# Kernel optimization log

Measured on AMD Instinct MI355X. Metric: run time of the kernel, lower is better.

## Reference

```python
import jax, jax.numpy as jnp
import numpy as np

CAPACITY = 8_388_608  # 2**23, power of two -> leftmost_leaf == capacity
N_UPDATES = 1_048_576  # 2**20


def setup_inputs() -> dict:
    key = jax.random.key(0)
    k1, k2, k3 = jax.random.split(key, 3)
    # Existing tree buffer; values[1] is root, values[CAPACITY:2*CAPACITY] are leaves.
    tree_values = jax.random.uniform(k1, (2 * CAPACITY,), dtype=jnp.float32)
    # Distinct leaf indices in [0, CAPACITY): torch scatter-assign with duplicate
    # indices is nondeterministic, so the meaningful case is distinct indices.
    indices = jax.random.permutation(k2, CAPACITY)[:N_UPDATES].astype(jnp.int32)
    values = jax.random.uniform(k3, (N_UPDATES,), dtype=jnp.float32)
    return {"tree_values": tree_values, "indices": indices, "values": values}


def reference(tree_values, indices, values):
    """SegmentTree.__setitem__ with op=add: set leaves, propagate sums to root.

    Returns the updated (2*capacity,) tree buffer.
    """
    capacity = tree_values.shape[0] // 2  # static python int
    depth = int(capacity).bit_length() - 1  # log2(capacity) levels to the root
    # _index_to_leaf: with power-of-two capacity, leaf = idx + capacity (no wrap).
    leaf = indices.astype(jnp.int32) + capacity
    tree = tree_values.at[leaf].set(values)
    idx = leaf
    # Original does torch.unique(idx//2) per level purely as an optimization;
    # duplicate parents recompute the identical value, so plain scatter-set of
    # op(left_child, right_child) is the same math and jit-friendly.
    for _ in range(depth):
        idx = idx // 2
        parent = tree[2 * idx] + tree[2 * idx + 1]
        tree = tree.at[idx].set(parent)
    return tree
```

## Files before the change

### kernel.cpp

```cpp
#include <hip/hip_runtime.h>


typedef unsigned int uint;
typedef unsigned char uchar;

__global__ void scatter_kernel(const int* __restrict__ idx,
                               const float* __restrict__ val,
                               float* __restrict__ overlay,
                               uchar* __restrict__ flags, int n) {
    int i = blockIdx.x * blockDim.x + threadIdx.x;
    if (i < n) {
        int j = idx[i];
        overlay[j] = val[i];
        flags[j] = 1;
    }
}

__global__ __launch_bounds__(256)
void merge_kernel(const float* __restrict__ tree,
                  const float* __restrict__ overlay,
                  const uchar* __restrict__ flags,
                  uchar* __restrict__ l11flag,
                  float* __restrict__ out, int C) {
    const int t = blockIdx.x * 256 + threadIdx.x;
    const int leaf0 = t * 8;

    const float4* tl = (const float4*)(tree + C + leaf0);
    float4 ta = tl[0], tb = tl[1];
    const float4* op = (const float4*)(overlay + leaf0);
    float4 oa = op[0], ob = op[1];
    uint2 f = *(const uint2*)(flags + leaf0);

    float l0 = (f.x & 0x000000FFu) ? oa.x : ta.x;
    float l1 = (f.x & 0x0000FF00u) ? oa.y : ta.y;
    float l2 = (f.x & 0x00FF0000u) ? oa.z : ta.z;
    float l3 = (f.x & 0xFF000000u) ? oa.w : ta.w;
    float l4 = (f.y & 0x000000FFu) ? ob.x : tb.x;
    float l5 = (f.y & 0x0000FF00u) ? ob.y : tb.y;
    float l6 = (f.y & 0x00FF0000u) ? ob.z : tb.z;
    float l7 = (f.y & 0xFF000000u) ? ob.w : tb.w;

    *(float4*)(out + C + leaf0)     = make_float4(l0, l1, l2, l3);
    *(float4*)(out + C + leaf0 + 4) = make_float4(l4, l5, l6, l7);

    uint d10 = (f.x & 0x0000FFFFu) != 0u;
    uint d11 = (f.x & 0xFFFF0000u) != 0u;
    uint d12 = (f.y & 0x0000FFFFu) != 0u;
    uint d13 = (f.y & 0xFFFF0000u) != 0u;
    float4 t1 = *(const float4*)(tree + (C >> 1) + 4 * t);
    float4 v1;
    v1.x = d10 ? l0 + l1 : t1.x;
    v1.y = d11 ? l2 + l3 : t1.y;
    v1.z = d12 ? l4 + l5 : t1.z;
    v1.w = d13 ? l6 + l7 : t1.w;
    *(float4*)(out + (C >> 1) + 4 * t) = v1;

    float2 t2 = *(const float2*)(tree + (C >> 2) + 2 * t);
    uint d20 = d10 | d11, d21 = d12 | d13;
    float2 v2;
    v2.x = d20 ? v1.x + v1.y : t2.x;
    v2.y = d21 ? v1.z + v1.w : t2.y;
    *(float2*)(out + (C >> 2) + 2 * t) = v2;

    float t3 = tree[(C >> 3) + t];
    uint d3 = d20 | d21;
    float v3 = d3 ? v2.x + v2.y : t3;
    out[(C >> 3) + t] = v3;

    __shared__ float sv[256];
    __shared__ uint  sd[256];
    float curv = v3;
    uint  curd = d3;
    const int nb = blockIdx.x * 2048;
    for (int lvl = 4; lvl <= 11; ++lvl) {
        sv[threadIdx.x] = curv;
        sd[threadIdx.x] = curd;
        __syncthreads();
        const int A = 2048 >> lvl;
        float nv = 0.f;
        uint  nd = 0u;
        if (threadIdx.x < A) {
            uint da = sd[2 * threadIdx.x], db = sd[2 * threadIdx.x + 1];
            nd = da | db;
            int node = (C >> lvl) + (nb >> lvl) + threadIdx.x;
            float tv = tree[node];
            nv = nd ? sv[2 * threadIdx.x] + sv[2 * threadIdx.x + 1] : tv;
            out[node] = nv;
        }
        __syncthreads();
        curv = nv;
        curd = nd;
    }
    if (threadIdx.x == 0) l11flag[blockIdx.x] = (uchar)curd;
}

__global__ __launch_bounds__(1024)
void tail_kernel(const float* __restrict__ tree,
                 const uchar* __restrict__ l11flag,
                 float* __restrict__ out) {
    __shared__ float va[2048];
    __shared__ uint  da[2048];
    const int tid = threadIdx.x;
    for (int i = tid; i < 2048; i += 1024) {
        int p = 2048 + i;
        uint nd = (uint)l11flag[2 * i] | (uint)l11flag[2 * i + 1];
        float v = nd ? out[2 * p] + out[2 * p + 1] : tree[p];
        out[p] = v;
        va[i] = v;
        da[i] = nd;
    }
    __syncthreads();
    for (int M = 1024; M >= 1; M >>= 1) {
        float v = 0.f;
        uint  nd = 0u;
        if (tid < M) {
            int p = M + tid;
            nd = da[2 * tid] | da[2 * tid + 1];
            v = nd ? va[2 * tid] + va[2 * tid + 1] : tree[p];
            out[p] = v;
        }
        __syncthreads();
        if (tid < M) { va[tid] = v; da[tid] = nd; }
        __syncthreads();
    }
    if (tid == 0) out[0] = tree[0];
}

extern "C" void kernel_launch(void* const* d_in, const int* in_sizes, int n_in,
                              void* d_out, int out_size, void* d_ws, size_t ws_size,
                              hipStream_t stream) {
    const float* tree    = (const float*)d_in[0];
    const int*   indices = (const int*)d_in[1];
    const float* values  = (const float*)d_in[2];
    float* out = (float*)d_out;

    const int two_cap = in_sizes[0];
    const int C       = two_cap >> 1;
    const int n_upd   = in_sizes[1];

    float* overlay = (float*)d_ws;
    uchar* flags   = (uchar*)d_ws + (size_t)C * 4;
    uchar* l11     = flags + C;

    hipMemsetAsync(flags, 0, (size_t)C, stream);

    scatter_kernel<<<(n_upd + 255) / 256, 256, 0, stream>>>(indices, values,
                                                            overlay, flags, n_upd);

    merge_kernel<<<C / 2048, 256, 0, stream>>>(tree, overlay, flags, l11, out, C);

    tail_kernel<<<1, 1024, 0, stream>>>(tree, l11, out);
}
```

Before: 165.5 us.

## Replace byte flags and overlay with bitmap and scatter directly into output

Replaces the per-leaf byte flag array with a 1-bit-per-leaf bitmap set by atomicOr, and scatters new leaf values straight into the output buffer instead of a separate overlay. The merge kernel reads one flag byte per 8 leaves and reads the overlay from the output's leaf region, which cuts flag traffic by 8x and removes the separate overlay array. The memset is replaced by a small clear kernel. In exchange the scatter uses atomics, and the merge kernel reads the output region it is also writing, though each thread reads only its own leaves before overwriting them.

```diff
diff --git a/kernel.cpp b/kernel.cpp
--- a/kernel.cpp
+++ b/kernel.cpp
@@ -4,49 +4,55 @@
 typedef unsigned int uint;
 typedef unsigned char uchar;
 
+__global__ void clear_kernel(uint4* __restrict__ bm4, int n4) {
+    int i = blockIdx.x * blockDim.x + threadIdx.x;
+    if (i < n4) bm4[i] = make_uint4(0u, 0u, 0u, 0u);
+}
+
 __global__ void scatter_kernel(const int* __restrict__ idx,
                                const float* __restrict__ val,
-                               float* __restrict__ overlay,
-                               uchar* __restrict__ flags, int n) {
+                               float* __restrict__ out,
+                               uint* __restrict__ bm,
+                               int C, int n) {
     int i = blockIdx.x * blockDim.x + threadIdx.x;
     if (i < n) {
         int j = idx[i];
-        overlay[j] = val[i];
-        flags[j] = 1;
+        out[C + j] = val[i];
+        atomicOr(&bm[j >> 5], 1u << (j & 31));
     }
 }
 
 __global__ __launch_bounds__(256)
 void merge_kernel(const float* __restrict__ tree,
-                  const float* __restrict__ overlay,
-                  const uchar* __restrict__ flags,
+                  const uint* __restrict__ bm,
                   uchar* __restrict__ l11flag,
                   float* __restrict__ out, int C) {
     const int t = blockIdx.x * 256 + threadIdx.x;
     const int leaf0 = t * 8;
 
+    uint f = ((const uchar*)bm)[t];
+
     const float4* tl = (const float4*)(tree + C + leaf0);
     float4 ta = tl[0], tb = tl[1];
-    const float4* op = (const float4*)(overlay + leaf0);
-    float4 oa = op[0], ob = op[1];
-    uint2 f = *(const uint2*)(flags + leaf0);
+    const float4* ol = (const float4*)(out + C + leaf0);
+    float4 oa = ol[0], ob = ol[1];
 
-    float l0 = (f.x & 0x000000FFu) ? oa.x : ta.x;
-    float l1 = (f.x & 0x0000FF00u) ? oa.y : ta.y;
-    float l2 = (f.x & 0x00FF0000u) ? oa.z : ta.z;
-    float l3 = (f.x & 0xFF000000u) ? oa.w : ta.w;
-    float l4 = (f.y & 0x000000FFu) ? ob.x : tb.x;
-    float l5 = (f.y & 0x0000FF00u) ? ob.y : tb.y;
-    float l6 = (f.y & 0x00FF0000u) ? ob.z : tb.z;
-    float l7 = (f.y & 0xFF000000u) ? ob.w : tb.w;
+    float l0 = (f & 0x01u) ? oa.x : ta.x;
+    float l1 = (f & 0x02u) ? oa.y : ta.y;
+    float l2 = (f & 0x04u) ? oa.z : ta.z;
+    float l3 = (f & 0x08u) ? oa.w : ta.w;
+    float l4 = (f & 0x10u) ? ob.x : tb.x;
+    float l5 = (f & 0x20u) ? ob.y : tb.y;
+    float l6 = (f & 0x40u) ? ob.z : tb.z;
+    float l7 = (f & 0x80u) ? ob.w : tb.w;
 
     *(float4*)(out + C + leaf0)     = make_float4(l0, l1, l2, l3);
     *(float4*)(out + C + leaf0 + 4) = make_float4(l4, l5, l6, l7);
 
-    uint d10 = (f.x & 0x0000FFFFu) != 0u;
-    uint d11 = (f.x & 0xFFFF0000u) != 0u;
-    uint d12 = (f.y & 0x0000FFFFu) != 0u;
-    uint d13 = (f.y & 0xFFFF0000u) != 0u;
+    uint d10 = (f & 0x03u) != 0u;
+    uint d11 = (f & 0x0Cu) != 0u;
+    uint d12 = (f & 0x30u) != 0u;
+    uint d13 = (f & 0xC0u) != 0u;
     float4 t1 = *(const float4*)(tree + (C >> 1) + 4 * t);
     float4 v1;
     v1.x = d10 ? l0 + l1 : t1.x;
@@ -80,8 +86,7 @@
         float nv = 0.f;
         uint  nd = 0u;
         if (threadIdx.x < A) {
-            uint da = sd[2 * threadIdx.x], db = sd[2 * threadIdx.x + 1];
-            nd = da | db;
+            nd = sd[2 * threadIdx.x] | sd[2 * threadIdx.x + 1];
             int node = (C >> lvl) + (nb >> lvl) + threadIdx.x;
             float tv = tree[node];
             nv = nd ? sv[2 * threadIdx.x] + sv[2 * threadIdx.x + 1] : tv;
@@ -138,16 +143,16 @@
     const int C       = two_cap >> 1;
     const int n_upd   = in_sizes[1];
 
-    float* overlay = (float*)d_ws;
-    uchar* flags   = (uchar*)d_ws + (size_t)C * 4;
-    uchar* l11     = flags + C;
+    uint*  bm  = (uint*)d_ws;
+    uchar* l11 = (uchar*)d_ws + (size_t)(C >> 3);
 
-    hipMemsetAsync(flags, 0, (size_t)C, stream);
+    const int nbm4 = C >> 7;
+    clear_kernel<<<nbm4 / 256, 256, 0, stream>>>((uint4*)d_ws, nbm4);
 
     scatter_kernel<<<(n_upd + 255) / 256, 256, 0, stream>>>(indices, values,
-                                                            overlay, flags, n_upd);
+                                                            out, bm, C, n_upd);
 
-    merge_kernel<<<C / 2048, 256, 0, stream>>>(tree, overlay, flags, l11, out, C);
+    merge_kernel<<<C / 2048, 256, 0, stream>>>(tree, bm, l11, out, C);
 
     tail_kernel<<<1, 1024, 0, stream>>>(tree, l11, out);
 }
```

After: 176.7 us. 6.8% more time.
